# Performance work log

Hardware: AMD Instinct MI355X
Metric: run time of the kernel (lower is better)

The kernel has to match this reference:

```python
import jax, jax.numpy as jnp
import numpy as np

N = 50000       # num entities
F_IN = 256      # input feature dim
H = 128         # hidden_dim (= per-head dim, concat=False)
HEADS = 4
L = 3           # num_layers
T = 3           # num edge types
E = 250000      # edges per type
NEG = 0.2       # leaky_relu slope (module + GATv2 default)


def setup_inputs() -> dict:
    key = jax.random.key(0)
    ks = jax.random.split(key, 10)
    s = 0.05
    return {
        "feat": jax.random.normal(ks[0], (N, F_IN), jnp.float32),
        "emb_table": jax.random.normal(ks[1], (N, H), jnp.float32),
        "proj_w": jax.random.normal(ks[2], (F_IN, H), jnp.float32) * s,
        "proj_b": jnp.zeros((H,), jnp.float32),
        "ln_g": jnp.ones((H,), jnp.float32),
        "ln_b": jnp.zeros((H,), jnp.float32),
        "skip_w": jnp.ones((L,), jnp.float32),
        "Wl": jax.random.normal(ks[3], (L, T, H, HEADS * H), jnp.float32) * s,
        "Wr": jax.random.normal(ks[4], (L, T, H, HEADS * H), jnp.float32) * s,
        "att": jax.random.normal(ks[5], (L, T, HEADS, H), jnp.float32) * s,
        "bias": jnp.zeros((L, T, H), jnp.float32),
        "edge_src": jax.random.randint(ks[6], (T, E), 0, N, jnp.int64),
        "edge_dst": jax.random.randint(ks[7], (T, E), 0, N, jnp.int64),
    }


def _layer_norm(x, g, b):
    mu = jnp.mean(x, axis=-1, keepdims=True)
    var = jnp.mean(jnp.square(x - mu), axis=-1, keepdims=True)
    return (x - mu) * jax.lax.rsqrt(var + 1e-5) * g + b


def _l2norm(x):
    n = jnp.sqrt(jnp.sum(jnp.square(x), axis=-1, keepdims=True))
    return x / jnp.maximum(n, 1e-12)


def _gatv2(x, wl, wr, a, b, src, dst):
    # x: [N,H]; wl,wr: [H, HEADS*H]; a: [HEADS,H]; src/dst: [E]
    xl = (x @ wl).reshape(N, HEADS, H)
    xr = (x @ wr).reshape(N, HEADS, H)
    m = xl[src] + xr[dst]                                   # [E,HEADS,H]
    e = jnp.sum(a * jax.nn.leaky_relu(m, NEG), axis=-1)     # [E,HEADS]
    # segment softmax over incoming edges per destination node
    emax = jax.lax.stop_gradient(jax.ops.segment_max(e, dst, num_segments=N))
    ex = jnp.exp(e - emax[dst])
    den = jax.ops.segment_sum(ex, dst, num_segments=N)      # [N,HEADS]
    alpha = ex / (den[dst] + 1e-16)                         # [E,HEADS]
    out = jax.ops.segment_sum(alpha[:, :, None] * xl[src], dst, num_segments=N)
    return jnp.mean(out, axis=1) + b                        # concat=False -> head mean


def reference(feat, emb_table, proj_w, proj_b, ln_g, ln_b, skip_w,
              Wl, Wr, att, bias, edge_src, edge_dst):
    h = jax.nn.leaky_relu(_layer_norm(feat @ proj_w + proj_b, ln_g, ln_b), NEG)
    ne = _l2norm(emb_table)                                 # normalize(embedding(arange(N)))
    x0 = 0.7 * h + 0.5 * ne
    x = x0
    for i in range(L):
        # HeteroConv(aggr='mean') over edge types, all on node type 'entity'
        per_type = [
            _gatv2(x, Wl[i, t], Wr[i, t], att[i, t], bias[i, t],
                   edge_src[t], edge_dst[t])
            for t in range(T)
        ]
        xu = jnp.mean(jnp.stack(per_type, axis=0), axis=0)
        alpha = jax.nn.sigmoid(skip_w[i])
        x = jax.nn.leaky_relu(xu, NEG) + alpha * x0          # dropout = identity (eval)
    return x
```

## Files before the change

### kernel.cpp

```cpp
#include <hip/hip_runtime.h>
#include <hip/hip_bf16.h>
#include <math.h>

#define N_NODES 50000
#define NOFF    50004
#define NBLK    49
#define F_IN    256
#define H       128
#define HEADS   4
#define HH      512
#define L_LAYERS 3
#define T_TYPES  3
#define E_EDGES  250000
#define NEG      0.2f

#define GEMM_RB  391
#define GEMM_GRID (GEMM_RB*8)

typedef __attribute__((ext_vector_type(8))) short short8_t;
typedef __attribute__((ext_vector_type(4))) float float4_t;
typedef __attribute__((ext_vector_type(2))) float float2_t;

__device__ __forceinline__ float leaky(float x) { return x > 0.f ? x : NEG * x; }

__device__ __forceinline__ unsigned int cvt_pk_bf16(float lo, float hi) {
    unsigned int d;
    asm("v_cvt_pk_bf16_f32 %0, %1, %2" : "=v"(d) : "v"(lo), "v"(hi));
    return d;
}

__device__ __forceinline__ unsigned short f2bf(float f) {
    return (unsigned short)cvt_pk_bf16(f, f);
}

__device__ __forceinline__ float bf2f(unsigned short u) {
    union { unsigned int i; float f; } v; v.i = ((unsigned)u) << 16; return v.f;
}

__device__ __forceinline__ float2_t pk_add(float2_t a, float2_t b) {
    float2_t d;
    asm("v_pk_add_f32 %0, %1, %2" : "=v"(d) : "v"(a), "v"(b));
    return d;
}
__device__ __forceinline__ float2_t pk_fma(float2_t a, float2_t b, float2_t c) {
    float2_t d;
    asm("v_pk_fma_f32 %0, %1, %2, %3" : "=v"(d) : "v"(a), "v"(b), "v"(c));
    return d;
}
__device__ __forceinline__ float2_t pk_abs(float2_t a) {
    union { float2_t f; unsigned int u[2]; } v; v.f = a;
    v.u[0] &= 0x7fffffffu;
    v.u[1] &= 0x7fffffffu;
    return v.f;
}

__device__ __forceinline__ float fast_exp2(float x) {
    return __builtin_amdgcn_exp2f(x);
}

template <int CTRL>
__device__ __forceinline__ float dpp_add(float x) {
    union { float f; int i; } a, b;
    a.f = x;
    b.i = __builtin_amdgcn_update_dpp(0, a.i, CTRL, 0xf, 0xf, true);
    return x + b.f;
}
__device__ __forceinline__ float row16_reduce(float p) {
    p = dpp_add<0xB1>(p);
    p = dpp_add<0x4E>(p);
    p = dpp_add<0x141>(p);
    p = dpp_add<0x140>(p);
    return p;
}

__device__ __forceinline__ void unpack_pk(uint4 q, float2_t* o) {
    union { unsigned int i; float f; } v;
    float2_t t;
    v.i = q.x << 16;         t.x = v.f;
    v.i = q.x & 0xffff0000u; t.y = v.f; o[0] = t;
    v.i = q.y << 16;         t.x = v.f;
    v.i = q.y & 0xffff0000u; t.y = v.f; o[1] = t;
    v.i = q.z << 16;         t.x = v.f;
    v.i = q.z & 0xffff0000u; t.y = v.f; o[2] = t;
    v.i = q.w << 16;         t.x = v.f;
    v.i = q.w & 0xffff0000u; t.y = v.f; o[3] = t;
}

__global__ void detect_kernel(const int* __restrict__ edst, int* __restrict__ flag) {
    __shared__ int s_any;
    if (threadIdx.x == 0) s_any = 0;
    __syncthreads();
    int a = 0;
    #pragma unroll
    for (int j = 0; j < 8; ++j) a |= edst[2 * (threadIdx.x * 8 + j) + 1];
    if (a) atomicOr(&s_any, 1);
    __syncthreads();
    if (threadIdx.x == 0) *flag = s_any ? 0 : 1;
}

__global__ void hist_kernel(const int* __restrict__ edst, int* __restrict__ counts,
                            const int* __restrict__ flag) {
    int idx = blockIdx.x * 256 + threadIdx.x;
    if (idx < T_TYPES * E_EDGES) {
        int sh = *flag;
        int t = idx / E_EDGES;
        int d = edst[(size_t)idx << sh];
        if ((unsigned)d < N_NODES)
            atomicAdd(&counts[t * N_NODES + d], 1);
    }
}

__global__ __launch_bounds__(256) void scan_a_kernel(const int* __restrict__ counts,
                                                     int* __restrict__ bsum) {
    const int b = blockIdx.x;
    const int t = b / NBLK, ch = b % NBLK;
    const int tid = threadIdx.x, lane = tid & 63;
    __shared__ int ws[4];
    const int* cnt = counts + t * N_NODES;
    int i0 = ch * 1024 + tid * 4;
    int s = 0;
    if (i0 + 3 < N_NODES) { int4 v = *(const int4*)(cnt + i0); s = v.x + v.y + v.z + v.w; }
    else { for (int j = 0; j < 4; ++j) { int i = i0 + j; if (i < N_NODES) s += cnt[i]; } }
    #pragma unroll
    for (int o = 32; o > 0; o >>= 1) s += __shfl_xor(s, o);
    if (lane == 0) ws[tid >> 6] = s;
    __syncthreads();
    if (tid == 0) bsum[b] = ws[0] + ws[1] + ws[2] + ws[3];
}

__global__ void scan_b_kernel(int* __restrict__ bsum, int* __restrict__ off) {
    int t = threadIdx.x;
    if (t < T_TYPES) {
        int run = 0;
        for (int c = 0; c < NBLK; ++c) { int v = bsum[t * NBLK + c]; bsum[t * NBLK + c] = run; run += v; }
        off[t * NOFF + N_NODES] = run;
    }
}

__global__ __launch_bounds__(256) void scan_c_kernel(const int* counts,
                                                     const int* __restrict__ bsum,
                                                     int* __restrict__ off,
                                                     int* cursor) {
    const int b = blockIdx.x;
    const int t = b / NBLK, ch = b % NBLK;
    const int tid = threadIdx.x, lane = tid & 63, w = tid >> 6;
    __shared__ int ws[4];
    const int* cnt = counts + t * N_NODES;
    int i0 = ch * 1024 + tid * 4;
    int v0 = 0, v1 = 0, v2 = 0, v3 = 0;
    if (i0 + 3 < N_NODES) { int4 v = *(const int4*)(cnt + i0); v0 = v.x; v1 = v.y; v2 = v.z; v3 = v.w; }
    else {
        if (i0     < N_NODES) v0 = cnt[i0];
        if (i0 + 1 < N_NODES) v1 = cnt[i0 + 1];
        if (i0 + 2 < N_NODES) v2 = cnt[i0 + 2];
        if (i0 + 3 < N_NODES) v3 = cnt[i0 + 3];
    }
    int s = v0 + v1 + v2 + v3;
    int x = s;
    #pragma unroll
    for (int o = 1; o < 64; o <<= 1) { int y = __shfl_up(x, o); if (lane >= o) x += y; }
    if (lane == 63) ws[w] = x;
    __syncthreads();
    int woff = 0;
    #pragma unroll
    for (int j = 0; j < 4; ++j) woff += (j < w) ? ws[j] : 0;
    int base = bsum[b] + woff + (x - s);
    int e0 = base, e1 = e0 + v0, e2 = e1 + v1, e3 = e2 + v2;
    if (i0 + 3 < N_NODES) {
        *(int4*)(off + t * NOFF + i0)       = make_int4(e0, e1, e2, e3);
        *(int4*)(cursor + t * N_NODES + i0) = make_int4(e0, e1, e2, e3);
    } else {
        if (i0     < N_NODES) { off[t * NOFF + i0]     = e0; cursor[t * N_NODES + i0]     = e0; }
        if (i0 + 1 < N_NODES) { off[t * NOFF + i0 + 1] = e1; cursor[t * N_NODES + i0 + 1] = e1; }
        if (i0 + 2 < N_NODES) { off[t * NOFF + i0 + 2] = e2; cursor[t * N_NODES + i0 + 2] = e2; }
        if (i0 + 3 < N_NODES) { off[t * NOFF + i0 + 3] = e3; cursor[t * N_NODES + i0 + 3] = e3; }
    }
}

__global__ void scatter_kernel(const int* __restrict__ esrc, const int* __restrict__ edst,
                               int* __restrict__ cursor, int* __restrict__ csrc,
                               const int* __restrict__ flag) {
    int idx = blockIdx.x * 256 + threadIdx.x;
    if (idx < T_TYPES * E_EDGES) {
        int sh = *flag;
        int t = idx / E_EDGES;
        int d = edst[(size_t)idx << sh];
        if ((unsigned)d >= N_NODES) return;
        int s = esrc[(size_t)idx << sh];
        if ((unsigned)s >= N_NODES) s = 0;
        int pos = atomicAdd(&cursor[t * N_NODES + d], 1);
        if ((unsigned)pos < E_EDGES)
            csrc[(size_t)t * E_EDGES + pos] = s;
    }
}

__global__ void wconv_kernel(const float* __restrict__ Wl, const float* __restrict__ Wr,
                             unsigned short* __restrict__ Wt) {
    int idx = blockIdx.x * 256 + threadIdx.x;
    if (idx >= L_LAYERS * T_TYPES * 1024 * H) return;
    int lt  = idx / (1024 * H);
    int rem = idx - lt * (1024 * H);
    int c   = rem / H;
    int k   = rem - c * H;
    float v = (c < HH) ? Wl[(size_t)lt * H * HH + (size_t)k * HH + c]
                       : Wr[(size_t)lt * H * HH + (size_t)k * HH + (c - HH)];
    Wt[idx] = f2bf(v);
}

__global__ void featconv_kernel(const float* __restrict__ feat,
                                unsigned short* __restrict__ fHi,
                                unsigned short* __restrict__ fLo) {
    size_t i = ((size_t)blockIdx.x * 256 + threadIdx.x) * 4;
    if (i >= (size_t)N_NODES * F_IN) return;
    float4 v = *(const float4*)(feat + i);
    ushort4 h, l;
    h.x = f2bf(v.x); l.x = f2bf(v.x - bf2f(h.x));
    h.y = f2bf(v.y); l.y = f2bf(v.y - bf2f(h.y));
    h.z = f2bf(v.z); l.z = f2bf(v.z - bf2f(h.z));
    h.w = f2bf(v.w); l.w = f2bf(v.w - bf2f(h.w));
    *(ushort4*)(fHi + i) = h;
    *(ushort4*)(fLo + i) = l;
}

__global__ void pconv_kernel(const float* __restrict__ pw,
                             unsigned short* __restrict__ pWtHi,
                             unsigned short* __restrict__ pWtLo) {
    int idx = blockIdx.x * 256 + threadIdx.x;
    if (idx >= H * F_IN) return;
    int c = idx / F_IN, k = idx - c * F_IN;
    float v = pw[(size_t)k * H + c];
    unsigned short hi = f2bf(v);
    pWtHi[idx] = hi;
    pWtLo[idx] = f2bf(v - bf2f(hi));
}

__device__ __forceinline__ void stage_tile(unsigned short* dst, const unsigned short* src,
                                           int rbase, int kbase, int tid, bool guardRows) {
    #pragma unroll
    for (int it = 0; it < 8; ++it) {
        int c = it * 256 + tid;
        int r = c >> 4, k8 = c & 15;
        int slot = (k8 ^ (r & 15)) * 8;
        uint4 v = make_uint4(0, 0, 0, 0);
        int row = rbase + r;
        if (!guardRows || row < N_NODES)
            v = *(const uint4*)(src + (size_t)row * 256 + kbase + k8 * 8);
        *(uint4*)(dst + r * 128 + slot) = v;
    }
}

__global__ __launch_bounds__(256) void init_gemm_kernel(
    const unsigned short* __restrict__ fHi, const unsigned short* __restrict__ fLo,
    const unsigned short* __restrict__ pWtHi, const unsigned short* __restrict__ pWtLo,
    float* __restrict__ proj)
{
    __shared__ unsigned short smem[32768];
    unsigned short* As = smem;
    unsigned short* Bs = smem + 16384;
    const int tid = threadIdx.x;
    const int nb = blockIdx.x * 128;

    const int wv = tid >> 6, lane = tid & 63;
    const int lm = lane & 15, kg = lane >> 4;
    const int wm = (wv & 1) * 64, wn = (wv >> 1) * 64;
    float4_t acc[4][4];
    #pragma unroll
    for (int i = 0; i < 4; ++i)
        #pragma unroll
        for (int j = 0; j < 4; ++j)
            acc[i][j] = (float4_t){0.f, 0.f, 0.f, 0.f};

    auto compute = [&]() {
        #pragma unroll
        for (int ks = 0; ks < 4; ++ks) {
            const int K8 = ks * 4 + kg;
            const int slot = (K8 ^ lm) * 8;
            short8_t a[4], b[4];
            #pragma unroll
            for (int i = 0; i < 4; ++i) {
                a[i] = *(const short8_t*)(As + (wm + i * 16 + lm) * 128 + slot);
                b[i] = *(const short8_t*)(Bs + (wn + i * 16 + lm) * 128 + slot);
            }
            #pragma unroll
            for (int i = 0; i < 4; ++i)
                #pragma unroll
                for (int j = 0; j < 4; ++j)
                    acc[i][j] = __builtin_amdgcn_mfma_f32_16x16x32_bf16(a[i], b[j], acc[i][j], 0, 0, 0);
        }
    };

    #pragma unroll
    for (int kh = 0; kh < 2; ++kh) {
        const int kbase = kh * 128;
        stage_tile(As, fHi, nb, kbase, tid, true);
        stage_tile(Bs, pWtHi, 0, kbase, tid, false);
        __syncthreads();
        compute();
        __syncthreads();
        stage_tile(Bs, pWtLo, 0, kbase, tid, false);
        __syncthreads();
        compute();
        __syncthreads();
        stage_tile(As, fLo, nb, kbase, tid, true);
        stage_tile(Bs, pWtHi, 0, kbase, tid, false);
        __syncthreads();
        compute();
        __syncthreads();
    }

    #pragma unroll
    for (int i = 0; i < 4; ++i) {
        #pragma unroll
        for (int r = 0; r < 4; ++r) {
            int node = nb + wm + i * 16 + kg * 4 + r;
            if (node < N_NODES) {
                #pragma unroll
                for (int j = 0; j < 4; ++j)
                    proj[(size_t)node * H + wn + j * 16 + lm] = acc[i][j][r];
            }
        }
    }
}

__global__ __launch_bounds__(128) void ln_combine_kernel(
    const float* __restrict__ proj, const float* __restrict__ emb,
    const float* __restrict__ pb, const float* __restrict__ g, const float* __restrict__ b,
    float* __restrict__ x0, unsigned short* __restrict__ xcurb)
{
    __shared__ float s0[2], s1[2];
    const int tid = threadIdx.x;
    const int nb = blockIdx.x * 8;
    const int c = tid;
    float acc[8];
    #pragma unroll
    for (int nn = 0; nn < 8; ++nn) {
        int node = nb + nn;
        acc[nn] = (node < N_NODES) ? proj[(size_t)node * H + c] : 0.f;
    }
    const float pbc = pb[c], gc = g[c], bc = b[c];
    for (int nn = 0; nn < 8; ++nn) {
        float v = acc[nn] + pbc;
        float sum = v, sq = v * v;
        for (int o = 32; o > 0; o >>= 1) { sum += __shfl_down(sum, o); sq += __shfl_down(sq, o); }
        if ((tid & 63) == 0) { s0[tid >> 6] = sum; s1[tid >> 6] = sq; }
        __syncthreads();
        float tot = s0[0] + s0[1], tq = s1[0] + s1[1];
        __syncthreads();
        float mu = tot * (1.f / H);
        float var = tq * (1.f / H) - mu * mu;
        acc[nn] = leaky((v - mu) * rsqrtf(var + 1e-5f) * gc + bc);
    }
    for (int nn = 0; nn < 8; ++nn) {
        int node = nb + nn;
        float ev = (node < N_NODES) ? emb[(size_t)node * H + c] : 0.f;
        float sq = ev * ev;
        for (int o = 32; o > 0; o >>= 1) sq += __shfl_down(sq, o);
        if ((tid & 63) == 0) s0[tid >> 6] = sq;
        __syncthreads();
        float nrm = sqrtf(s0[0] + s0[1]);
        __syncthreads();
        float nev = ev / fmaxf(nrm, 1e-12f);
        float xv = 0.7f * acc[nn] + 0.5f * nev;
        if (node < N_NODES) {
            x0[(size_t)node * H + c] = xv;
            xcurb[(size_t)node * H + c] = f2bf(xv);
        }
    }
}

__global__ __launch_bounds__(256) void gemm_mfma_kernel(
    const unsigned short* __restrict__ x,
    const unsigned short* __restrict__ Wt,
    unsigned short* __restrict__ XL, unsigned short* __restrict__ XR)
{
    __shared__ unsigned short smem[32768];
    unsigned short* As = smem;
    unsigned short* Bs = smem + 16384;
    const int tid = threadIdx.x;

    const int f    = blockIdx.x;
    const int g    = (f % 8) * GEMM_RB + (f / 8);
    const int rowb = g >> 3;
    const int colb = g & 7;
    const int nb = rowb * 128;
    const int cb = colb * 128;

    #pragma unroll
    for (int it = 0; it < 8; ++it) {
        int c = it * 256 + tid;
        int r = c >> 4;
        int k8 = c & 15;
        int slot = (k8 ^ (r & 15)) * 8;
        int node = nb + r;
        uint4 va = make_uint4(0, 0, 0, 0);
        if (node < N_NODES) va = *(const uint4*)(x + (size_t)node * H + k8 * 8);
        *(uint4*)(As + r * H + slot) = va;
        uint4 vb = *(const uint4*)(Wt + (size_t)(cb + r) * H + k8 * 8);
        *(uint4*)(Bs + r * H + slot) = vb;
    }
    __syncthreads();

    const int wv = tid >> 6, lane = tid & 63;
    const int lm = lane & 15, kg = lane >> 4;
    const int wm = (wv & 1) * 64, wn = (wv >> 1) * 64;
    float4_t acc[4][4];
    #pragma unroll
    for (int i = 0; i < 4; ++i)
        #pragma unroll
        for (int j = 0; j < 4; ++j)
            acc[i][j] = (float4_t){0.f, 0.f, 0.f, 0.f};

    #pragma unroll
    for (int ks = 0; ks < 4; ++ks) {
        const int K8 = ks * 4 + kg;
        const int slot = (K8 ^ lm) * 8;
        short8_t a[4], b[4];
        #pragma unroll
        for (int i = 0; i < 4; ++i) {
            a[i] = *(const short8_t*)(As + (wm + i * 16 + lm) * H + slot);
            b[i] = *(const short8_t*)(Bs + (wn + i * 16 + lm) * H + slot);
        }
        #pragma unroll
        for (int i = 0; i < 4; ++i)
            #pragma unroll
            for (int j = 0; j < 4; ++j)
                acc[i][j] = __builtin_amdgcn_mfma_f32_16x16x32_bf16(a[i], b[j], acc[i][j], 0, 0, 0);
    }
    __syncthreads();

    unsigned short* Cs = smem;
    #pragma unroll
    for (int i = 0; i < 4; ++i) {
        int row0 = wm + i * 16 + kg * 4;
        #pragma unroll
        for (int j = 0; j < 4; ++j) {
            int col = wn + j * 16 + lm;
            #pragma unroll
            for (int r = 0; r < 4; ++r)
                Cs[(row0 + r) * 136 + col] = f2bf(acc[i][j][r]);
        }
    }
    __syncthreads();

    unsigned short* O = (colb < 4) ? XL : XR;
    const int cbase = (colb < 4) ? cb : cb - HH;
    #pragma unroll
    for (int it = 0; it < 8; ++it) {
        int c = it * 256 + tid;
        int r = c >> 4, k8 = (c & 15) * 8;
        int node = nb + r;
        if (node < N_NODES)
            *(uint4*)(O + (size_t)node * HH + cbase + k8) = *(const uint4*)(Cs + r * 136 + k8);
    }
}

__global__ __launch_bounds__(64) void aggregate_kernel(
    const unsigned short* __restrict__ XL, const unsigned short* __restrict__ XR,
    const float* __restrict__ att_t, const float* __restrict__ bias_t,
    const int* __restrict__ off, const int* __restrict__ csrc,
    float* __restrict__ xacc, int first,
    int fin, const float* __restrict__ x0, const float* __restrict__ skipw,
    int li, int last, unsigned short* __restrict__ xcurb, float* __restrict__ out)
{
    const int lane = threadIdx.x;
    const int d = blockIdx.x;
    if (d >= N_NODES) return;
    const int jb = lane * 8;
    const float L2E = 1.4426950408889634f;

    float2_t rv[4], c1[4], c2[4], acc2[4];
    {
        uint4 q = *(const uint4*)(XR + (size_t)d * HH + jb);
        unpack_pk(q, rv);
        float4 u0 = *(const float4*)(att_t + jb);
        float4 u1 = *(const float4*)(att_t + jb + 4);
        float av[8] = {u0.x, u0.y, u0.z, u0.w, u1.x, u1.y, u1.z, u1.w};
        #pragma unroll
        for (int u = 0; u < 4; ++u) {
            c1[u] = (float2_t){0.6f * L2E * av[2 * u], 0.6f * L2E * av[2 * u + 1]};
            c2[u] = (float2_t){0.4f * L2E * av[2 * u], 0.4f * L2E * av[2 * u + 1]};
            acc2[u] = (float2_t){0.f, 0.f};
        }
    }
    float den = 0.f;

    const int e0 = off[d];
    const int cnt = off[d + 1] - e0;

    uint4 q0 = make_uint4(0, 0, 0, 0), q1 = q0;
    unsigned s2 = 0, s3 = 0;
    if (cnt > 0) q0 = *(const uint4*)(XL + (size_t)((unsigned)csrc[e0])     * HH + jb);
    if (cnt > 1) q1 = *(const uint4*)(XL + (size_t)((unsigned)csrc[e0 + 1]) * HH + jb);
    if (cnt > 2) s2 = (unsigned)csrc[e0 + 2];
    if (cnt > 3) s3 = (unsigned)csrc[e0 + 3];

    int e = 0;
    for (; e + 1 < cnt; e += 2) {
        float2_t lv0[4], lv1[4];
        unpack_pk(q0, lv0);
        unpack_pk(q1, lv1);
        if (e + 2 < cnt) q0 = *(const uint4*)(XL + (size_t)s2 * HH + jb);
        if (e + 3 < cnt) q1 = *(const uint4*)(XL + (size_t)s3 * HH + jb);
        if (e + 4 < cnt) s2 = (unsigned)csrc[e0 + e + 4];
        if (e + 5 < cnt) s3 = (unsigned)csrc[e0 + e + 5];

        float2_t p20 = (float2_t){0.f, 0.f};
        float2_t p21 = (float2_t){0.f, 0.f};
        #pragma unroll
        for (int u = 0; u < 4; ++u) {
            float2_t m0 = pk_add(lv0[u], rv[u]);
            float2_t m1 = pk_add(lv1[u], rv[u]);
            float2_t a0 = pk_abs(m0);
            float2_t a1 = pk_abs(m1);
            p20 = pk_fma(c1[u], m0, p20);
            p21 = pk_fma(c1[u], m1, p21);
            p20 = pk_fma(c2[u], a0, p20);
            p21 = pk_fma(c2[u], a1, p21);
        }
        float p0 = row16_reduce(p20.x + p20.y);
        float p1 = row16_reduce(p21.x + p21.y);
        float w0 = fast_exp2(p0);
        float w1 = fast_exp2(p1);
        den += w0 + w1;
        float2_t w20 = (float2_t){w0, w0};
        float2_t w21 = (float2_t){w1, w1};
        #pragma unroll
        for (int u = 0; u < 4; ++u) {
            acc2[u] = pk_fma(w20, lv0[u], acc2[u]);
            acc2[u] = pk_fma(w21, lv1[u], acc2[u]);
        }
    }
    if (e < cnt) {
        float2_t lv0[4];
        unpack_pk(q0, lv0);
        float2_t p20 = (float2_t){0.f, 0.f};
        #pragma unroll
        for (int u = 0; u < 4; ++u) {
            float2_t m0 = pk_add(lv0[u], rv[u]);
            float2_t a0 = pk_abs(m0);
            p20 = pk_fma(c1[u], m0, p20);
            p20 = pk_fma(c2[u], a0, p20);
        }
        float p0 = row16_reduce(p20.x + p20.y);
        float w0 = fast_exp2(p0);
        den += w0;
        float2_t w20 = (float2_t){w0, w0};
        #pragma unroll
        for (int u = 0; u < 4; ++u) acc2[u] = pk_fma(w20, lv0[u], acc2[u]);
    }

    float inv = 1.f / (den + 1e-16f);
    float o[8];
    #pragma unroll
    for (int u = 0; u < 4; ++u) { o[2 * u] = acc2[u].x; o[2 * u + 1] = acc2[u].y; }
    #pragma unroll
    for (int u = 0; u < 8; ++u) {
        float v = o[u] * inv;
        v += __shfl_xor(v, 16);
        v += __shfl_xor(v, 32);
        o[u] = v * 0.25f;
    }
    if (lane < 16) {
        float* dst = xacc + (size_t)d * H + jb;
        #pragma unroll
        for (int u = 0; u < 8; ++u) o[u] += bias_t[jb + u];
        if (!fin) {
            float4 o0 = make_float4(o[0], o[1], o[2], o[3]);
            float4 o1 = make_float4(o[4], o[5], o[6], o[7]);
            if (first) {
                *(float4*)dst = o0;
                *(float4*)(dst + 4) = o1;
            } else {
                float4 c0 = *(const float4*)dst, c1v = *(const float4*)(dst + 4);
                o0.x += c0.x; o0.y += c0.y; o0.z += c0.z; o0.w += c0.w;
                o1.x += c1v.x; o1.y += c1v.y; o1.z += c1v.z; o1.w += c1v.w;
                *(float4*)dst = o0;
                *(float4*)(dst + 4) = o1;
            }
        } else {
            float sw = 1.f / (1.f + __expf(-skipw[li]));
            float4 c0 = *(const float4*)dst, c1v = *(const float4*)(dst + 4);
            float a0 = c0.x + o[0], a1 = c0.y + o[1], a2 = c0.z + o[2], a3 = c0.w + o[3];
            float a4 = c1v.x + o[4], a5 = c1v.y + o[5], a6 = c1v.z + o[6], a7 = c1v.w + o[7];
            const float* z = x0 + (size_t)d * H + jb;
            float4 z0 = *(const float4*)z, z1 = *(const float4*)(z + 4);
            float r0 = leaky(a0 * (1.f / 3.f)) + sw * z0.x;
            float r1 = leaky(a1 * (1.f / 3.f)) + sw * z0.y;
            float r2 = leaky(a2 * (1.f / 3.f)) + sw * z0.z;
            float r3 = leaky(a3 * (1.f / 3.f)) + sw * z0.w;
            float r4 = leaky(a4 * (1.f / 3.f)) + sw * z1.x;
            float r5 = leaky(a5 * (1.f / 3.f)) + sw * z1.y;
            float r6 = leaky(a6 * (1.f / 3.f)) + sw * z1.z;
            float r7 = leaky(a7 * (1.f / 3.f)) + sw * z1.w;
            if (last) {
                float* op = out + (size_t)d * H + jb;
                *(float4*)op       = make_float4(r0, r1, r2, r3);
                *(float4*)(op + 4) = make_float4(r4, r5, r6, r7);
            } else {
                unsigned int w0 = cvt_pk_bf16(r0, r1);
                unsigned int w1 = cvt_pk_bf16(r2, r3);
                unsigned int w2 = cvt_pk_bf16(r4, r5);
                unsigned int w3 = cvt_pk_bf16(r6, r7);
                *(uint4*)(xcurb + (size_t)d * H + jb) = make_uint4(w0, w1, w2, w3);
            }
        }
    }
}

extern "C" void kernel_launch(void* const* d_in, const int* in_sizes, int n_in,
                              void* d_out, int out_size, void* d_ws, size_t ws_size,
                              hipStream_t stream)
{
    const float* feat   = (const float*)d_in[0];
    const float* emb    = (const float*)d_in[1];
    const float* proj_w = (const float*)d_in[2];
    const float* proj_b = (const float*)d_in[3];
    const float* ln_g   = (const float*)d_in[4];
    const float* ln_b   = (const float*)d_in[5];
    const float* skip_w = (const float*)d_in[6];
    const float* Wl     = (const float*)d_in[7];
    const float* Wr     = (const float*)d_in[8];
    const float* att    = (const float*)d_in[9];
    const float* bias   = (const float*)d_in[10];
    const int*   esrc   = (const int*)d_in[11];
    const int*   edst   = (const int*)d_in[12];
    float* out = (float*)d_out;

    char* p = (char*)d_ws;
    auto alloc = [&](size_t bytes) -> char* {
        char* r = p; p += (bytes + 255) & ~(size_t)255; return r;
    };
    float* x0             = (float*)alloc((size_t)N_NODES * H * 4);
    unsigned short* xcurb = (unsigned short*)alloc((size_t)N_NODES * H * 2);
    unsigned short* XL    = (unsigned short*)alloc((size_t)N_NODES * HH * 2);
    unsigned short* XR    = (unsigned short*)alloc((size_t)N_NODES * HH * 2);
    unsigned short* Wt    = (unsigned short*)alloc((size_t)L_LAYERS * T_TYPES * 1024 * H * 2);
    unsigned short* pWtHi = (unsigned short*)alloc((size_t)H * F_IN * 2);
    unsigned short* pWtLo = (unsigned short*)alloc((size_t)H * F_IN * 2);
    int* off    = (int*)alloc((size_t)T_TYPES * NOFF * 4);
    int* cursor = (int*)alloc((size_t)T_TYPES * N_NODES * 4);
    int* csrc   = (int*)alloc((size_t)T_TYPES * E_EDGES * 4);
    int* bsum   = (int*)alloc((size_t)T_TYPES * NBLK * 4);
    int* eflag  = (int*)alloc(256);
    float* xacc = out;

    float* proj          = (float*)XL;
    unsigned short* fHi  = XR;
    unsigned short* fLo  = XR + (size_t)N_NODES * F_IN;

    detect_kernel<<<1, 256, 0, stream>>>(edst, eflag);
    hipMemsetAsync(cursor, 0, (size_t)T_TYPES * N_NODES * 4, stream);
    hist_kernel<<<(T_TYPES * E_EDGES + 255) / 256, 256, 0, stream>>>(edst, cursor, eflag);
    scan_a_kernel<<<T_TYPES * NBLK, 256, 0, stream>>>(cursor, bsum);
    scan_b_kernel<<<1, 256, 0, stream>>>(bsum, off);
    scan_c_kernel<<<T_TYPES * NBLK, 256, 0, stream>>>(cursor, bsum, off, cursor);
    scatter_kernel<<<(T_TYPES * E_EDGES + 255) / 256, 256, 0, stream>>>(esrc, edst, cursor, csrc, eflag);

    wconv_kernel<<<(L_LAYERS * T_TYPES * 1024 * H + 255) / 256, 256, 0, stream>>>(Wl, Wr, Wt);
    featconv_kernel<<<((N_NODES * F_IN / 4) + 255) / 256, 256, 0, stream>>>(feat, fHi, fLo);
    pconv_kernel<<<(H * F_IN + 255) / 256, 256, 0, stream>>>(proj_w, pWtHi, pWtLo);
    init_gemm_kernel<<<(N_NODES + 127) / 128, 256, 0, stream>>>(fHi, fLo, pWtHi, pWtLo, proj);
    ln_combine_kernel<<<N_NODES / 8, 128, 0, stream>>>(proj, emb, proj_b, ln_g, ln_b, x0, xcurb);

    for (int i = 0; i < L_LAYERS; ++i) {
        for (int t = 0; t < T_TYPES; ++t) {
            const int lt = i * T_TYPES + t;
            const unsigned short* wt = Wt + (size_t)lt * 1024 * H;
            const float* at = att + (size_t)lt * HEADS * H;
            const float* bi = bias + (size_t)lt * H;
            gemm_mfma_kernel<<<GEMM_GRID, 256, 0, stream>>>(xcurb, wt, XL, XR);
            aggregate_kernel<<<N_NODES, 64, 0, stream>>>(
                XL, XR, at, bi, off + t * NOFF, csrc + (size_t)t * E_EDGES,
                xacc, (t == 0) ? 1 : 0,
                (t == T_TYPES - 1) ? 1 : 0, x0, skip_w, i,
                (i == L_LAYERS - 1) ? 1 : 0, xcurb, out);
        }
    }
}
```

Before: 1.095 ms.

## Fuse per-type GEMM and aggregation across edge types within each layer

Adds a GEMM kernel that computes XL/XR for all three edge types of a layer in one launch, writing into per-type buffers. Adds an aggregate kernel that processes all three edge types per destination node and keeps the sum in registers, removing the global xacc accumulation and the separate finalize step. The fused path needs three times the XL/XR workspace, so it is enabled only when the workspace is large enough; otherwise the old per-type path is used. The larger intermediates may lose cache residency between GEMM and aggregation.

```diff
diff --git a/kernel.cpp b/kernel.cpp
--- a/kernel.cpp
+++ b/kernel.cpp
@@ -14,8 +14,9 @@
 #define E_EDGES  250000
 #define NEG      0.2f
 
-#define GEMM_RB  391
+#define GEMM_RB   391
 #define GEMM_GRID (GEMM_RB*8)
+#define GEMM_GRID_F (GEMM_RB*24)
 
 typedef __attribute__((ext_vector_type(8))) short short8_t;
 typedef __attribute__((ext_vector_type(4))) float float4_t;
@@ -368,21 +369,14 @@
     }
 }
 
-__global__ __launch_bounds__(256) void gemm_mfma_kernel(
-    const unsigned short* __restrict__ x,
-    const unsigned short* __restrict__ Wt,
-    unsigned short* __restrict__ XL, unsigned short* __restrict__ XR)
+__device__ __forceinline__ void gemm_tile_body(
+    const unsigned short* __restrict__ x, const unsigned short* __restrict__ Wtt,
+    unsigned short* __restrict__ XLt, unsigned short* __restrict__ XRt,
+    int nb, int colb, int tid)
 {
     __shared__ unsigned short smem[32768];
     unsigned short* As = smem;
     unsigned short* Bs = smem + 16384;
-    const int tid = threadIdx.x;
-
-    const int f    = blockIdx.x;
-    const int g    = (f % 8) * GEMM_RB + (f / 8);
-    const int rowb = g >> 3;
-    const int colb = g & 7;
-    const int nb = rowb * 128;
     const int cb = colb * 128;
 
     #pragma unroll
@@ -395,7 +389,7 @@
         uint4 va = make_uint4(0, 0, 0, 0);
         if (node < N_NODES) va = *(const uint4*)(x + (size_t)node * H + k8 * 8);
         *(uint4*)(As + r * H + slot) = va;
-        uint4 vb = *(const uint4*)(Wt + (size_t)(cb + r) * H + k8 * 8);
+        uint4 vb = *(const uint4*)(Wtt + (size_t)(cb + r) * H + k8 * 8);
         *(uint4*)(Bs + r * H + slot) = vb;
     }
     __syncthreads();
@@ -442,7 +436,7 @@
     }
     __syncthreads();
 
-    unsigned short* O = (colb < 4) ? XL : XR;
+    unsigned short* O = (colb < 4) ? XLt : XRt;
     const int cbase = (colb < 4) ? cb : cb - HH;
     #pragma unroll
     for (int it = 0; it < 8; ++it) {
@@ -454,20 +448,40 @@
     }
 }
 
-__global__ __launch_bounds__(64) void aggregate_kernel(
+__global__ __launch_bounds__(256) void gemm_mfma_kernel(
+    const unsigned short* __restrict__ x, const unsigned short* __restrict__ Wt,
+    unsigned short* __restrict__ XL, unsigned short* __restrict__ XR)
+{
+    const int f    = blockIdx.x;
+    const int g    = (f % 8) * GEMM_RB + (f / 8);
+    const int rowb = g >> 3;
+    const int colb = g & 7;
+    gemm_tile_body(x, Wt, XL, XR, rowb * 128, colb, threadIdx.x);
+}
+
+__global__ __launch_bounds__(256) void gemm_mfma_fused_kernel(
+    const unsigned short* __restrict__ x,
+    const unsigned short* __restrict__ Wt_l,
+    unsigned short* __restrict__ XLall, unsigned short* __restrict__ XRall)
+{
+    const int f    = blockIdx.x;
+    const int g    = (f % 8) * (GEMM_RB * 3) + (f / 8);
+    const int rowb = g / 24;
+    const int c24  = g % 24;
+    const int type = c24 >> 3;
+    const int colb = c24 & 7;
+    const unsigned short* Wtt = Wt_l + (size_t)type * 1024 * H;
+    unsigned short* XLt = XLall + (size_t)type * N_NODES * HH;
+    unsigned short* XRt = XRall + (size_t)type * N_NODES * HH;
+    gemm_tile_body(x, Wtt, XLt, XRt, rowb * 128, colb, threadIdx.x);
+}
+
+__device__ __forceinline__ void agg_one_type(
     const unsigned short* __restrict__ XL, const unsigned short* __restrict__ XR,
-    const float* __restrict__ att_t, const float* __restrict__ bias_t,
-    const int* __restrict__ off, const int* __restrict__ csrc,
-    float* __restrict__ xacc, int first,
-    int fin, const float* __restrict__ x0, const float* __restrict__ skipw,
-    int li, int last, unsigned short* __restrict__ xcurb, float* __restrict__ out)
-{
-    const int lane = threadIdx.x;
-    const int d = blockIdx.x;
-    if (d >= N_NODES) return;
-    const int jb = lane * 8;
+    const float* __restrict__ att_t, const int* __restrict__ off, const int* __restrict__ csrc,
+    int d, int jb, float2_t* s2)
+{
     const float L2E = 1.4426950408889634f;
-
     float2_t rv[4], c1[4], c2[4], acc2[4];
     {
         uint4 q = *(const uint4*)(XR + (size_t)d * HH + jb);
@@ -488,21 +502,21 @@
     const int cnt = off[d + 1] - e0;
 
     uint4 q0 = make_uint4(0, 0, 0, 0), q1 = q0;
-    unsigned s2 = 0, s3 = 0;
+    unsigned s2i = 0, s3i = 0;
     if (cnt > 0) q0 = *(const uint4*)(XL + (size_t)((unsigned)csrc[e0])     * HH + jb);
     if (cnt > 1) q1 = *(const uint4*)(XL + (size_t)((unsigned)csrc[e0 + 1]) * HH + jb);
-    if (cnt > 2) s2 = (unsigned)csrc[e0 + 2];
-    if (cnt > 3) s3 = (unsigned)csrc[e0 + 3];
+    if (cnt > 2) s2i = (unsigned)csrc[e0 + 2];
+    if (cnt > 3) s3i = (unsigned)csrc[e0 + 3];
 
     int e = 0;
     for (; e + 1 < cnt; e += 2) {
         float2_t lv0[4], lv1[4];
         unpack_pk(q0, lv0);
         unpack_pk(q1, lv1);
-        if (e + 2 < cnt) q0 = *(const uint4*)(XL + (size_t)s2 * HH + jb);
-        if (e + 3 < cnt) q1 = *(const uint4*)(XL + (size_t)s3 * HH + jb);
-        if (e + 4 < cnt) s2 = (unsigned)csrc[e0 + e + 4];
-        if (e + 5 < cnt) s3 = (unsigned)csrc[e0 + e + 5];
+        if (e + 2 < cnt) q0 = *(const uint4*)(XL + (size_t)s2i * HH + jb);
+        if (e + 3 < cnt) q1 = *(const uint4*)(XL + (size_t)s3i * HH + jb);
+        if (e + 4 < cnt) s2i = (unsigned)csrc[e0 + e + 4];
+        if (e + 5 < cnt) s3i = (unsigned)csrc[e0 + e + 5];
 
         float2_t p20 = (float2_t){0.f, 0.f};
         float2_t p21 = (float2_t){0.f, 0.f};
@@ -550,12 +564,35 @@
     }
 
     float inv = 1.f / (den + 1e-16f);
+    float2_t inv2 = (float2_t){inv, inv};
+    #pragma unroll
+    for (int u = 0; u < 4; ++u) s2[u] = pk_fma(inv2, acc2[u], s2[u]);
+}
+
+__global__ __launch_bounds__(64) void aggregate_kernel(
+    const unsigned short* __restrict__ XL, const unsigned short* __restrict__ XR,
+    const float* __restrict__ att_t, const float* __restrict__ bias_t,
+    const int* __restrict__ off, const int* __restrict__ csrc,
+    float* __restrict__ xacc, int first,
+    int fin, const float* __restrict__ x0, const float* __restrict__ skipw,
+    int li, int last, unsigned short* __restrict__ xcurb, float* __restrict__ out)
+{
+    const int lane = threadIdx.x;
+    const int d = blockIdx.x;
+    if (d >= N_NODES) return;
+    const int jb = lane * 8;
+
+    float2_t s2[4];
+    #pragma unroll
+    for (int u = 0; u < 4; ++u) s2[u] = (float2_t){0.f, 0.f};
+    agg_one_type(XL, XR, att_t, off, csrc, d, jb, s2);
+
     float o[8];
     #pragma unroll
-    for (int u = 0; u < 4; ++u) { o[2 * u] = acc2[u].x; o[2 * u + 1] = acc2[u].y; }
+    for (int u = 0; u < 4; ++u) { o[2 * u] = s2[u].x; o[2 * u + 1] = s2[u].y; }
     #pragma unroll
     for (int u = 0; u < 8; ++u) {
-        float v = o[u] * inv;
+        float v = o[u];
         v += __shfl_xor(v, 16);
         v += __shfl_xor(v, 32);
         o[u] = v * 0.25f;
@@ -607,6 +644,69 @@
     }
 }
 
+__global__ __launch_bounds__(64) void aggregate_fused_kernel(
+    const unsigned short* __restrict__ XLall, const unsigned short* __restrict__ XRall,
+    const float* __restrict__ att_l,
+    const float* __restrict__ bias_l,
+    const int* __restrict__ off,
+    const int* __restrict__ csrc,
+    const float* __restrict__ x0, const float* __restrict__ skipw,
+    int li, int last, unsigned short* __restrict__ xcurb, float* __restrict__ out)
+{
+    const int lane = threadIdx.x;
+    const int d = blockIdx.x;
+    if (d >= N_NODES) return;
+    const int jb = lane * 8;
+
+    float2_t s2[4];
+    #pragma unroll
+    for (int u = 0; u < 4; ++u) s2[u] = (float2_t){0.f, 0.f};
+
+    for (int t = 0; t < T_TYPES; ++t) {
+        agg_one_type(XLall + (size_t)t * N_NODES * HH,
+                     XRall + (size_t)t * N_NODES * HH,
+                     att_l + (size_t)t * HH,
+                     off + (size_t)t * NOFF,
+                     csrc + (size_t)t * E_EDGES,
+                     d, jb, s2);
+    }
+
+    float o[8];
+    #pragma unroll
+    for (int u = 0; u < 4; ++u) { o[2 * u] = s2[u].x; o[2 * u + 1] = s2[u].y; }
+    #pragma unroll
+    for (int u = 0; u < 8; ++u) {
+        float v = o[u];
+        v += __shfl_xor(v, 16);
+        v += __shfl_xor(v, 32);
+        o[u] = v * 0.25f;
+    }
+    if (lane < 16) {
+        const float sw = 1.f / (1.f + __expf(-skipw[li]));
+        const float* z = x0 + (size_t)d * H + jb;
+        float4 z0 = *(const float4*)z, z1 = *(const float4*)(z + 4);
+        float r[8];
+        #pragma unroll
+        for (int u = 0; u < 8; ++u) {
+            float bsum = bias_l[jb + u] + bias_l[H + jb + u] + bias_l[2 * H + jb + u];
+            float zu = (u < 4) ? ((u == 0) ? z0.x : (u == 1) ? z0.y : (u == 2) ? z0.z : z0.w)
+                               : ((u == 4) ? z1.x : (u == 5) ? z1.y : (u == 6) ? z1.z : z1.w);
+            r[u] = leaky((o[u] + bsum) * (1.f / 3.f)) + sw * zu;
+        }
+        if (last) {
+            float* op = out + (size_t)d * H + jb;
+            *(float4*)op       = make_float4(r[0], r[1], r[2], r[3]);
+            *(float4*)(op + 4) = make_float4(r[4], r[5], r[6], r[7]);
+        } else {
+            unsigned int w0 = cvt_pk_bf16(r[0], r[1]);
+            unsigned int w1 = cvt_pk_bf16(r[2], r[3]);
+            unsigned int w2 = cvt_pk_bf16(r[4], r[5]);
+            unsigned int w3 = cvt_pk_bf16(r[6], r[7]);
+            *(uint4*)(xcurb + (size_t)d * H + jb) = make_uint4(w0, w1, w2, w3);
+        }
+    }
+}
+
 extern "C" void kernel_launch(void* const* d_in, const int* in_sizes, int n_in,
                               void* d_out, int out_size, void* d_ws, size_t ws_size,
                               hipStream_t stream)
@@ -626,14 +726,17 @@
     const int*   edst   = (const int*)d_in[12];
     float* out = (float*)d_out;
 
+    const bool fused = ws_size >= ((size_t)370 << 20);
+    const int NPAIR = fused ? T_TYPES : 1;
+
     char* p = (char*)d_ws;
     auto alloc = [&](size_t bytes) -> char* {
         char* r = p; p += (bytes + 255) & ~(size_t)255; return r;
     };
     float* x0             = (float*)alloc((size_t)N_NODES * H * 4);
     unsigned short* xcurb = (unsigned short*)alloc((size_t)N_NODES * H * 2);
-    unsigned short* XL    = (unsigned short*)alloc((size_t)N_NODES * HH * 2);
-    unsigned short* XR    = (unsigned short*)alloc((size_t)N_NODES * HH * 2);
+    unsigned short* XL    = (unsigned short*)alloc((size_t)NPAIR * N_NODES * HH * 2);
+    unsigned short* XR    = (unsigned short*)alloc((size_t)NPAIR * N_NODES * HH * 2);
     unsigned short* Wt    = (unsigned short*)alloc((size_t)L_LAYERS * T_TYPES * 1024 * H * 2);
     unsigned short* pWtHi = (unsigned short*)alloc((size_t)H * F_IN * 2);
     unsigned short* pWtLo = (unsigned short*)alloc((size_t)H * F_IN * 2);
@@ -662,18 +765,30 @@
     init_gemm_kernel<<<(N_NODES + 127) / 128, 256, 0, stream>>>(fHi, fLo, pWtHi, pWtLo, proj);
     ln_combine_kernel<<<N_NODES / 8, 128, 0, stream>>>(proj, emb, proj_b, ln_g, ln_b, x0, xcurb);
 
-    for (int i = 0; i < L_LAYERS; ++i) {
-        for (int t = 0; t < T_TYPES; ++t) {
-            const int lt = i * T_TYPES + t;
-            const unsigned short* wt = Wt + (size_t)lt * 1024 * H;
-            const float* at = att + (size_t)lt * HEADS * H;
-            const float* bi = bias + (size_t)lt * H;
-            gemm_mfma_kernel<<<GEMM_GRID, 256, 0, stream>>>(xcurb, wt, XL, XR);
-            aggregate_kernel<<<N_NODES, 64, 0, stream>>>(
-                XL, XR, at, bi, off + t * NOFF, csrc + (size_t)t * E_EDGES,
-                xacc, (t == 0) ? 1 : 0,
-                (t == T_TYPES - 1) ? 1 : 0, x0, skip_w, i,
+    if (fused) {
+        for (int i = 0; i < L_LAYERS; ++i) {
+            const unsigned short* wt_l = Wt + (size_t)i * T_TYPES * 1024 * H;
+            const float* at_l = att + (size_t)i * T_TYPES * HEADS * H;
+            const float* bi_l = bias + (size_t)i * T_TYPES * H;
+            gemm_mfma_fused_kernel<<<GEMM_GRID_F, 256, 0, stream>>>(xcurb, wt_l, XL, XR);
+            aggregate_fused_kernel<<<N_NODES, 64, 0, stream>>>(
+                XL, XR, at_l, bi_l, off, csrc, x0, skip_w, i,
                 (i == L_LAYERS - 1) ? 1 : 0, xcurb, out);
         }
-    }
-}
+    } else {
+        for (int i = 0; i < L_LAYERS; ++i) {
+            for (int t = 0; t < T_TYPES; ++t) {
+                const int lt = i * T_TYPES + t;
+                const unsigned short* wt = Wt + (size_t)lt * 1024 * H;
+                const float* at = att + (size_t)lt * HEADS * H;
+                const float* bi = bias + (size_t)lt * H;
+                gemm_mfma_kernel<<<GEMM_GRID, 256, 0, stream>>>(xcurb, wt, XL, XR);
+                aggregate_kernel<<<N_NODES, 64, 0, stream>>>(
+                    XL, XR, at, bi, off + t * NOFF, csrc + (size_t)t * E_EDGES,
+                    xacc, (t == 0) ? 1 : 0,
+                    (t == T_TYPES - 1) ? 1 : 0, x0, skip_w, i,
+                    (i == L_LAYERS - 1) ? 1 : 0, xcurb, out);
+            }
+        }
+    }
+}
```

Result: no change. 1.096 ms (+0.1%).
